# Kernel tuning notes

Measured on AMD Instinct MI355X. Metric: run time of the kernel, lower is better.

## Reference

```python
import jax, jax.numpy as jnp
import numpy as np

B, S, D, E = 4, 4096, 2048, 8


def setup_inputs() -> dict:
    key = jax.random.key(0)
    kx, kw, kb = jax.random.split(key, 3)
    x = jax.random.normal(kx, (B, S, D), dtype=jnp.float32)
    # nn.Linear(d_model, n_experts): weight [E, D], bias [E]
    bound = 1.0 / np.sqrt(D)
    W = jax.random.uniform(kw, (E, D), minval=-bound, maxval=bound, dtype=jnp.float32)
    b = jax.random.uniform(kb, (E,), minval=-bound, maxval=bound, dtype=jnp.float32)
    return {"x": x, "W": W, "b": b}


def reference(x, W, b):
    # logits = x @ W^T + b : [B, S, E]
    logits = jnp.einsum("bsd,ed->bse", x, W) + b
    gate = jax.nn.softmax(logits, axis=-1)
    top2_val, top2_idx = jax.lax.top_k(gate, 2)  # [B, S, 2] each
    return (top2_val, top2_idx, gate)
```

## Files before the change

kernel.cpp:

```cpp
#include <hip/hip_runtime.h>
#include <hip/hip_bf16.h>
#include <math.h>


#define NTOK   16384
#define DM     2048
#define NE     8

__device__ __forceinline__ float fold4(const float4 a) {
    return (a.x + a.y) + (a.z + a.w);
}

__device__ __forceinline__ float reduce_scatter8(const float4* acc, const int j) {
    float v0 = fold4(acc[0]), v1 = fold4(acc[1]), v2 = fold4(acc[2]), v3 = fold4(acc[3]);
    float v4 = fold4(acc[4]), v5 = fold4(acc[5]), v6 = fold4(acc[6]), v7 = fold4(acc[7]);
    float s0 = v0 + __shfl_xor(v0, 1, 8);
    float s1 = v1 + __shfl_xor(v1, 1, 8);
    float s2 = v2 + __shfl_xor(v2, 1, 8);
    float s3 = v3 + __shfl_xor(v3, 1, 8);
    float s4 = v4 + __shfl_xor(v4, 1, 8);
    float s5 = v5 + __shfl_xor(v5, 1, 8);
    float s6 = v6 + __shfl_xor(v6, 1, 8);
    float s7 = v7 + __shfl_xor(v7, 1, 8);
    const bool b0 = (j & 1);
    float t0 = b0 ? s1 : s0;
    float t1 = b0 ? s3 : s2;
    float t2 = b0 ? s5 : s4;
    float t3 = b0 ? s7 : s6;
    float p0 = t0 + __shfl_xor(t0, 2, 8);
    float p1 = t1 + __shfl_xor(t1, 2, 8);
    float p2 = t2 + __shfl_xor(t2, 2, 8);
    float p3 = t3 + __shfl_xor(t3, 2, 8);
    const bool b1 = (j & 2);
    float u0 = b1 ? p1 : p0;
    float u1 = b1 ? p3 : p2;
    float q0 = u0 + __shfl_xor(u0, 4, 8);
    float q1 = u1 + __shfl_xor(u1, 4, 8);
    return (j & 4) ? q1 : q0;
}

__device__ __forceinline__ void softmax_top2(const float logit, const int j,
                                             const int token, float* __restrict__ out) {
    float m = logit;
#pragma unroll
    for (int s = 4; s; s >>= 1) m = fmaxf(m, __shfl_xor(m, s, 8));
    const float ex = expf(logit - m);
    float sum = ex;
#pragma unroll
    for (int s = 4; s; s >>= 1) sum += __shfl_xor(sum, s, 8);
    const float gate = ex / sum;

    out[65536 + token * NE + j] = gate;

    float g1 = gate; int e1 = j;
#pragma unroll
    for (int s = 4; s; s >>= 1) {
        const float og = __shfl_xor(g1, s, 8);
        const int   oe = __shfl_xor(e1, s, 8);
        if (og > g1 || (og == g1 && oe < e1)) { g1 = og; e1 = oe; }
    }
    float g2 = (j == e1) ? -INFINITY : gate; int e2 = j;
#pragma unroll
    for (int s = 4; s; s >>= 1) {
        const float og = __shfl_xor(g2, s, 8);
        const int   oe = __shfl_xor(e2, s, 8);
        if (og > g2 || (og == g2 && oe < e2)) { g2 = og; e2 = oe; }
    }
    if (j == 0) {
        out[token * 2 + 0]         = g1;
        out[token * 2 + 1]         = g2;
        out[32768 + token * 2 + 0] = (float)e1;
        out[32768 + token * 2 + 1] = (float)e2;
    }
}

__device__ __forceinline__ void fma_group(const float* __restrict__ wbase,
                                          const float4 xa0, const float4 xa1,
                                          float4* __restrict__ acc0,
                                          float4* __restrict__ acc1) {
#pragma unroll
    for (int e = 0; e < NE; ++e) {
        const float4 wv = *reinterpret_cast<const float4*>(wbase + e * DM);
        acc0[e].x = fmaf(xa0.x, wv.x, acc0[e].x);
        acc0[e].y = fmaf(xa0.y, wv.y, acc0[e].y);
        acc0[e].z = fmaf(xa0.z, wv.z, acc0[e].z);
        acc0[e].w = fmaf(xa0.w, wv.w, acc0[e].w);
        acc1[e].x = fmaf(xa1.x, wv.x, acc1[e].x);
        acc1[e].y = fmaf(xa1.y, wv.y, acc1[e].y);
        acc1[e].z = fmaf(xa1.z, wv.z, acc1[e].z);
        acc1[e].w = fmaf(xa1.w, wv.w, acc1[e].w);
    }
}

__global__ __launch_bounds__(256, 1) void top2router_kernel(
    const float* __restrict__ x,
    const float* __restrict__ W,
    const float* __restrict__ b,
    float* __restrict__ out)
{
    __shared__ __align__(16) float sW[NE * DM];

    const int t = threadIdx.x;

    {
        const float4* __restrict__ Wv = reinterpret_cast<const float4*>(W);
        float4* sWv = reinterpret_cast<float4*>(sW);
#pragma unroll
        for (int i = 0; i < 16; ++i)
            sWv[i * 256 + t] = Wv[i * 256 + t];
    }
    __syncthreads();

    const int lane = t & 63;
    const int wave = t >> 6;
    const int j    = lane & 7;
    const int st   = lane >> 3;
    const int base = (blockIdx.x * 4 + wave) * 16;
    const int tok0 = base + st;
    const int tok1 = base + st + 8;

    const float* __restrict__ xp0 = x + (size_t)tok0 * DM + (j << 2);
    const float* __restrict__ xp1 = x + (size_t)tok1 * DM + (j << 2);
    const float bj = b[j];

    float4 acc0[NE], acc1[NE];
#pragma unroll
    for (int e = 0; e < NE; ++e) {
        acc0[e] = make_float4(0.f, 0.f, 0.f, 0.f);
        acc1[e] = make_float4(0.f, 0.f, 0.f, 0.f);
    }

    float4 pb0[4], pb1[4];
#pragma unroll
    for (int p = 0; p < 4; ++p) {
        pb0[p] = *reinterpret_cast<const float4*>(xp0 + (p << 5));
        pb1[p] = *reinterpret_cast<const float4*>(xp1 + (p << 5));
    }

#pragma unroll 3
    for (int kk = 0; kk < 60; kk += 4) {
        float4 cb0[4], cb1[4];
#pragma unroll
        for (int p = 0; p < 4; ++p) { cb0[p] = pb0[p]; cb1[p] = pb1[p]; }
#pragma unroll
        for (int p = 0; p < 4; ++p) {
            pb0[p] = *reinterpret_cast<const float4*>(xp0 + ((kk + 4 + p) << 5));
            pb1[p] = *reinterpret_cast<const float4*>(xp1 + ((kk + 4 + p) << 5));
        }
#pragma unroll
        for (int p = 0; p < 4; ++p)
            fma_group(&sW[((kk + p) << 5) + (j << 2)], cb0[p], cb1[p], acc0, acc1);
    }
#pragma unroll
    for (int p = 0; p < 4; ++p)
        fma_group(&sW[((60 + p) << 5) + (j << 2)], pb0[p], pb1[p], acc0, acc1);

    const float logit0 = reduce_scatter8(acc0, j) + bj;
    const float logit1 = reduce_scatter8(acc1, j) + bj;

    softmax_top2(logit0, j, tok0, out);
    softmax_top2(logit1, j, tok1, out);
}

extern "C" void kernel_launch(void* const* d_in, const int* in_sizes, int n_in,
                              void* d_out, int out_size, void* d_ws, size_t ws_size,
                              hipStream_t stream) {
    const float* x = (const float*)d_in[0];
    const float* W = (const float*)d_in[1];
    const float* b = (const float*)d_in[2];
    float* out = (float*)d_out;

    top2router_kernel<<<256, 256, 0, stream>>>(x, W, b, out);
}
```

Before: 194.8 us.

## Stage x tiles through double-buffered LDS with cooperative coalesced loads

Replaces per-thread direct global loads of x with a cooperative, contiguous load of 128-wide k-tiles for 64 tokens into a double-buffered shared-memory array. The next tile is prefetched into registers while the current tile is consumed from LDS. The aim is better coalescing of the x stream. In exchange it adds LDS traffic, 64 KB more shared memory, and a block barrier per tile.

```diff
diff --git a/kernel.cpp b/kernel.cpp
--- a/kernel.cpp
+++ b/kernel.cpp
@@ -3,9 +3,12 @@
 #include <math.h>
 
 
-#define NTOK   16384
-#define DM     2048
-#define NE     8
+#define NTOK  16384
+#define DM    2048
+#define NE    8
+#define KT    128
+#define NTILE (DM / KT)
+#define TPB   64
 
 __device__ __forceinline__ float fold4(const float4 a) {
     return (a.x + a.y) + (a.z + a.w);
@@ -74,24 +77,6 @@
     }
 }
 
-__device__ __forceinline__ void fma_group(const float* __restrict__ wbase,
-                                          const float4 xa0, const float4 xa1,
-                                          float4* __restrict__ acc0,
-                                          float4* __restrict__ acc1) {
-#pragma unroll
-    for (int e = 0; e < NE; ++e) {
-        const float4 wv = *reinterpret_cast<const float4*>(wbase + e * DM);
-        acc0[e].x = fmaf(xa0.x, wv.x, acc0[e].x);
-        acc0[e].y = fmaf(xa0.y, wv.y, acc0[e].y);
-        acc0[e].z = fmaf(xa0.z, wv.z, acc0[e].z);
-        acc0[e].w = fmaf(xa0.w, wv.w, acc0[e].w);
-        acc1[e].x = fmaf(xa1.x, wv.x, acc1[e].x);
-        acc1[e].y = fmaf(xa1.y, wv.y, acc1[e].y);
-        acc1[e].z = fmaf(xa1.z, wv.z, acc1[e].z);
-        acc1[e].w = fmaf(xa1.w, wv.w, acc1[e].w);
-    }
-}
-
 __global__ __launch_bounds__(256, 1) void top2router_kernel(
     const float* __restrict__ x,
     const float* __restrict__ W,
@@ -99,8 +84,17 @@
     float* __restrict__ out)
 {
     __shared__ __align__(16) float sW[NE * DM];
+    __shared__ __align__(16) float sX[2][TPB * KT];
 
-    const int t = threadIdx.x;
+    const int t    = threadIdx.x;
+    const int lane = t & 63;
+    const int wave = t >> 6;
+    const int j    = lane & 7;
+    const int st   = lane >> 3;
+    const int blk  = blockIdx.x;
+
+    const int half = lane >> 5;
+    const int hl   = lane & 31;
 
     {
         const float4* __restrict__ Wv = reinterpret_cast<const float4*>(W);
@@ -109,19 +103,21 @@
         for (int i = 0; i < 16; ++i)
             sWv[i * 256 + t] = Wv[i * 256 + t];
     }
+
+#pragma unroll
+    for (int i = 0; i < 8; ++i) {
+        const int c   = wave * 8 + i;
+        const int tok = 2 * c + half;
+        const float4 v = *reinterpret_cast<const float4*>(
+            x + (size_t)(blk * TPB + tok) * DM + hl * 4);
+        *reinterpret_cast<float4*>(&sX[0][tok * KT + hl * 4]) = v;
+    }
     __syncthreads();
 
-    const int lane = t & 63;
-    const int wave = t >> 6;
-    const int j    = lane & 7;
-    const int st   = lane >> 3;
-    const int base = (blockIdx.x * 4 + wave) * 16;
-    const int tok0 = base + st;
-    const int tok1 = base + st + 8;
-
-    const float* __restrict__ xp0 = x + (size_t)tok0 * DM + (j << 2);
-    const float* __restrict__ xp1 = x + (size_t)tok1 * DM + (j << 2);
-    const float bj = b[j];
+    const int t0    = wave * 16 + st;
+    const int t1    = t0 + 8;
+    const int gtok0 = blk * TPB + t0;
+    const int gtok1 = blk * TPB + t1;
 
     float4 acc0[NE], acc1[NE];
 #pragma unroll
@@ -130,36 +126,56 @@
         acc1[e] = make_float4(0.f, 0.f, 0.f, 0.f);
     }
 
-    float4 pb0[4], pb1[4];
+    int cur = 0;
+    for (int tl = 0; tl < NTILE; ++tl) {
+        float4 r[8];
+        if (tl + 1 < NTILE) {
 #pragma unroll
-    for (int p = 0; p < 4; ++p) {
-        pb0[p] = *reinterpret_cast<const float4*>(xp0 + (p << 5));
-        pb1[p] = *reinterpret_cast<const float4*>(xp1 + (p << 5));
+            for (int i = 0; i < 8; ++i) {
+                const int c   = wave * 8 + i;
+                const int tok = 2 * c + half;
+                r[i] = *reinterpret_cast<const float4*>(
+                    x + (size_t)(blk * TPB + tok) * DM + (tl + 1) * KT + hl * 4);
+            }
+        }
+
+#pragma unroll
+        for (int k2 = 0; k2 < KT / 32; ++k2) {
+            const int xo = k2 * 32 + j * 4;
+            const float4 xv0 = *reinterpret_cast<const float4*>(&sX[cur][t0 * KT + xo]);
+            const float4 xv1 = *reinterpret_cast<const float4*>(&sX[cur][t1 * KT + xo]);
+            const int wo = tl * KT + xo;
+#pragma unroll
+            for (int e = 0; e < NE; ++e) {
+                const float4 wv = *reinterpret_cast<const float4*>(&sW[e * DM + wo]);
+                acc0[e].x = fmaf(xv0.x, wv.x, acc0[e].x);
+                acc0[e].y = fmaf(xv0.y, wv.y, acc0[e].y);
+                acc0[e].z = fmaf(xv0.z, wv.z, acc0[e].z);
+                acc0[e].w = fmaf(xv0.w, wv.w, acc0[e].w);
+                acc1[e].x = fmaf(xv1.x, wv.x, acc1[e].x);
+                acc1[e].y = fmaf(xv1.y, wv.y, acc1[e].y);
+                acc1[e].z = fmaf(xv1.z, wv.z, acc1[e].z);
+                acc1[e].w = fmaf(xv1.w, wv.w, acc1[e].w);
+            }
+        }
+
+        if (tl + 1 < NTILE) {
+#pragma unroll
+            for (int i = 0; i < 8; ++i) {
+                const int c   = wave * 8 + i;
+                const int tok = 2 * c + half;
+                *reinterpret_cast<float4*>(&sX[cur ^ 1][tok * KT + hl * 4]) = r[i];
+            }
+        }
+        __syncthreads();
+        cur ^= 1;
     }
 
-#pragma unroll 3
-    for (int kk = 0; kk < 60; kk += 4) {
-        float4 cb0[4], cb1[4];
-#pragma unroll
-        for (int p = 0; p < 4; ++p) { cb0[p] = pb0[p]; cb1[p] = pb1[p]; }
-#pragma unroll
-        for (int p = 0; p < 4; ++p) {
-            pb0[p] = *reinterpret_cast<const float4*>(xp0 + ((kk + 4 + p) << 5));
-            pb1[p] = *reinterpret_cast<const float4*>(xp1 + ((kk + 4 + p) << 5));
-        }
-#pragma unroll
-        for (int p = 0; p < 4; ++p)
-            fma_group(&sW[((kk + p) << 5) + (j << 2)], cb0[p], cb1[p], acc0, acc1);
-    }
-#pragma unroll
-    for (int p = 0; p < 4; ++p)
-        fma_group(&sW[((60 + p) << 5) + (j << 2)], pb0[p], pb1[p], acc0, acc1);
+    const float logit0 = reduce_scatter8(acc0, j) + b[j];
+    const float logit1 = reduce_scatter8(acc1, j) + b[j];
 
-    const float logit0 = reduce_scatter8(acc0, j) + bj;
-    const float logit1 = reduce_scatter8(acc1, j) + bj;
-
-    softmax_top2(logit0, j, tok0, out);
-    softmax_top2(logit1, j, tok1, out);
+    softmax_top2(logit0, j, gtok0, out);
+    softmax_top2(logit1, j, gtok1, out);
 }
 
 extern "C" void kernel_launch(void* const* d_in, const int* in_sizes, int n_in,
@@ -170,5 +186,5 @@
     const float* b = (const float*)d_in[2];
     float* out = (float*)d_out;
 
-    top2router_kernel<<<256, 256, 0, stream>>>(x, W, b, out);
+    top2router_kernel<<<NTOK / TPB, 256, 0, stream>>>(x, W, b, out);
 }
```

New measurement: 196.1 us. No clear change (+0.6%).
